# Kernel optimization log

Hardware: AMD Instinct MI355X
Metric: run time of the kernel (lower is better)

The kernel has to match this reference:

```python
import jax, jax.numpy as jnp
import numpy as np

B, D, H, K = 65536, 256, 256, 11
TEMP = 1.0
EPS = 1e-8  # torch cosine_similarity eps


def _gelu(v):
    return jax.nn.gelu(v, approximate=False)  # torch nn.GELU default is exact


def setup_inputs() -> dict:
    key = jax.random.key(0)
    ks = jax.random.split(key, 9)
    s_d = 1.0 / np.sqrt(D)
    s_h = 1.0 / np.sqrt(H)
    return {
        "x": jax.random.normal(ks[0], (B, D), jnp.float32),
        # K transform MLPs, stacked: D->H (gelu) ->D
        "Tw1": jax.random.normal(ks[1], (K, D, H), jnp.float32) * s_d,
        "Tb1": jax.random.normal(ks[2], (K, H), jnp.float32) * 0.01,
        "Tw2": jax.random.normal(ks[3], (K, H, D), jnp.float32) * s_h,
        "Tb2": jax.random.normal(ks[4], (K, D), jnp.float32) * 0.01,
        # encoder MLP: D->H (gelu) ->H
        "Ew1": jax.random.normal(ks[5], (D, H), jnp.float32) * s_d,
        "Eb1": jax.random.normal(ks[6], (H,), jnp.float32) * 0.01,
        "Ew2": jax.random.normal(ks[7], (H, H), jnp.float32) * s_h,
        "Eb2": jax.random.normal(ks[8], (H,), jnp.float32) * 0.01,
    }


def reference(x, Tw1, Tb1, Tw2, Tb2, Ew1, Eb1, Ew2, Eb2):
    def enc(h):  # [..., D] -> [..., H]; dropout is identity at inference
        return _gelu(h @ Ew1 + Eb1) @ Ew2 + Eb2

    # batched transforms: [K, B, D]
    tx = _gelu(jnp.einsum('bd,kdh->kbh', x, Tw1) + Tb1[:, None, :])
    tx = jnp.einsum('kbh,khd->kbd', tx, Tw2) + Tb2[:, None, :]

    z = enc(x)        # [B, H]
    zt = enc(tx)      # [K, B, H]

    nz = jnp.linalg.norm(z, axis=-1)    # [B]
    nzt = jnp.linalg.norm(zt, axis=-1)  # [K, B]

    # exp(cos(z, z_k) / T)  -> [K, B]
    sim_z = jnp.exp(jnp.einsum('bh,kbh->kb', z, zt)
                    / jnp.maximum(nz[None, :] * nzt, EPS) / TEMP)
    # exp(cos(z_l, z_k) / T) -> [K, K, B]
    S = jnp.exp(jnp.einsum('lbh,kbh->lkb', zt, zt)
                / jnp.maximum(nzt[:, None, :] * nzt[None, :, :], EPS) / TEMP)
    diag = jnp.diagonal(S, axis1=0, axis2=1).T  # [K, B]
    neg = S.sum(axis=0) - diag                  # sum over l != k

    scores = jnp.log(sim_z / (sim_z + neg))     # [K, B]
    return -scores.sum(axis=0)                  # [B]
```

## Files before the change

### kernel.cpp

```cpp
#include <hip/hip_runtime.h>
#include <hip/hip_bf16.h>
#include <stdint.h>

#define BTOT  65536
#define KTR   11
#define NSLOT 12

typedef __attribute__((ext_vector_type(8))) short bf16x8_t;
typedef __attribute__((ext_vector_type(4))) float f32x4_t;

__device__ __forceinline__ int act_addr(int m, int n) {
    return m * 256 + ((((n >> 3) + m) & 31) << 3) + (n & 7);
}

__device__ __forceinline__ float gelu_fast(float x) {
    float x2 = x * x;
    float t2 = 1.5957691216057308f * x * fmaf(0.044715f, x2, 1.0f);
    float e  = __expf(fminf(t2, 30.f));
    return x * e * __builtin_amdgcn_rcpf(1.0f + e);
}

__global__ void cast_x_kernel(const float* __restrict__ x, __hip_bfloat16* __restrict__ xb) {
    int i = (blockIdx.x * 256 + threadIdx.x) * 4;
    float4 v = *(const float4*)(x + i);
    union { __hip_bfloat16 h[4]; uint64_t u; } o;
    o.h[0] = __float2bfloat16(v.x);
    o.h[1] = __float2bfloat16(v.y);
    o.h[2] = __float2bfloat16(v.z);
    o.h[3] = __float2bfloat16(v.w);
    *(uint64_t*)(xb + i) = o.u;
}

__global__ void transpose_cast_kernel(const float* __restrict__ in,
                                      __hip_bfloat16* __restrict__ out,
                                      int R, int C) {
    __shared__ float tile[32][33];
    int tpc = C >> 5;
    int tr = (blockIdx.x / tpc) << 5;
    int tc = (blockIdx.x % tpc) << 5;
    const float* bi = in + (size_t)blockIdx.y * R * C;
    __hip_bfloat16* bo = out + (size_t)blockIdx.y * R * C;
    int lx = threadIdx.x & 31, ly = threadIdx.x >> 5;
    #pragma unroll
    for (int r = 0; r < 32; r += 8)
        tile[ly + r][lx] = bi[(size_t)(tr + ly + r) * C + tc + lx];
    __syncthreads();
    #pragma unroll
    for (int r = 0; r < 32; r += 8)
        bo[(size_t)(tc + ly + r) * R + tr + lx] = __float2bfloat16(tile[lx][ly + r]);
}

__global__ void fuse_w_kernel(const __hip_bfloat16* __restrict__ Ew1t,
                              const __hip_bfloat16* __restrict__ Tw2b,
                              __hip_bfloat16* __restrict__ Wft)
{
    __shared__ __align__(16) __hip_bfloat16 bt[64 * 256];
    const int tid  = threadIdx.x;
    const int wave = tid >> 6, lane = tid & 63;
    const int lr = lane & 15, q = lane >> 4;
    const int k  = blockIdx.y;
    const int h0 = blockIdx.x << 6;
    const __hip_bfloat16* src = Tw2b + (size_t)k * 65536;

    #pragma unroll
    for (int i = 0; i < 8; ++i) {
        int lin = i * 256 + tid;
        int r = lin >> 5, g = lin & 31;
        bf16x8_t v = *(const bf16x8_t*)(src + (size_t)(h0 + r) * 256 + g * 8);
        *(bf16x8_t*)(bt + act_addr(r, g * 8)) = v;
    }
    __syncthreads();

    const int wc = wave << 6;
    f32x4_t acc[4][4];
    #pragma unroll
    for (int mt = 0; mt < 4; ++mt)
        #pragma unroll
        for (int nt = 0; nt < 4; ++nt)
            acc[mt][nt] = (f32x4_t){0.f, 0.f, 0.f, 0.f};

    #pragma unroll 1
    for (int kc = 0; kc < 8; ++kc) {
        const int kof = (kc << 5) + (q << 3);
        bf16x8_t a[4], b[4];
        #pragma unroll
        for (int mt = 0; mt < 4; ++mt)
            a[mt] = *(const bf16x8_t*)(Ew1t + (size_t)(wc + (mt << 4) + lr) * 256 + kof);
        #pragma unroll
        for (int nt = 0; nt < 4; ++nt)
            b[nt] = *(const bf16x8_t*)(bt + act_addr((nt << 4) + lr, kof));
        #pragma unroll
        for (int mt = 0; mt < 4; ++mt)
            #pragma unroll
            for (int nt = 0; nt < 4; ++nt)
                acc[mt][nt] = __builtin_amdgcn_mfma_f32_16x16x32_bf16(a[mt], b[nt], acc[mt][nt], 0, 0, 0);
    }

    __hip_bfloat16* dst = Wft + (size_t)k * 65536;
    #pragma unroll
    for (int mt = 0; mt < 4; ++mt)
        #pragma unroll
        for (int nt = 0; nt < 4; ++nt) {
            const int h = h0 + (nt << 4) + lr;
            #pragma unroll
            for (int r = 0; r < 4; ++r) {
                const int j = wc + (mt << 4) + (q << 2) + r;
                dst[(size_t)j * 256 + h] = __float2bfloat16(acc[mt][nt][r]);
            }
        }
}

__global__ void fuse_b_kernel(const float* __restrict__ Tb2,
                              const float* __restrict__ Ew1,
                              const float* __restrict__ Eb1,
                              float* __restrict__ bf)
{
    const int k = blockIdx.x, j = threadIdx.x;
    float s = Eb1[j];
    #pragma unroll 4
    for (int d = 0; d < 256; ++d)
        s = fmaf(Tb2[k * 256 + d], Ew1[d * 256 + j], s);
    bf[k * 256 + j] = s;
}

__device__ void run_stage(__hip_bfloat16* act,
                          const __hip_bfloat16* __restrict__ Wt,
                          const float* __restrict__ bias,
                          bool do_gelu, int wave, int lane)
{
    const int lr = lane & 15;
    const int q  = lane >> 4;
    const int wc = wave << 6;

    f32x4_t acc[4][4];
    #pragma unroll
    for (int mt = 0; mt < 4; ++mt)
        #pragma unroll
        for (int nt = 0; nt < 4; ++nt)
            acc[mt][nt] = (f32x4_t){0.f, 0.f, 0.f, 0.f};

    bf16x8_t a[4];
    #pragma unroll
    for (int mt = 0; mt < 4; ++mt)
        a[mt] = *(const bf16x8_t*)(Wt + (size_t)(wc + (mt << 4) + lr) * 256 + (q << 3));

    #pragma unroll 1
    for (int kc = 0; kc < 8; ++kc) {
        const int kof = (kc << 5) + (q << 3);
        bf16x8_t an[4];
        if (kc < 7) {
            #pragma unroll
            for (int mt = 0; mt < 4; ++mt)
                an[mt] = *(const bf16x8_t*)(Wt + (size_t)(wc + (mt << 4) + lr) * 256 + kof + 32);
        }
        bf16x8_t b[4];
        #pragma unroll
        for (int nt = 0; nt < 4; ++nt)
            b[nt] = *(const bf16x8_t*)(act + act_addr((nt << 4) + lr, kof));
        #pragma unroll
        for (int mt = 0; mt < 4; ++mt)
            #pragma unroll
            for (int nt = 0; nt < 4; ++nt)
                acc[mt][nt] = __builtin_amdgcn_mfma_f32_16x16x32_bf16(a[mt], b[nt], acc[mt][nt], 0, 0, 0);
        if (kc < 7) {
            #pragma unroll
            for (int mt = 0; mt < 4; ++mt) a[mt] = an[mt];
        }
    }

    __syncthreads();
    #pragma unroll
    for (int mt = 0; mt < 4; ++mt) {
        const int nbase = wc + (mt << 4) + (q << 2);
        const float4 bv = *(const float4*)(bias + nbase);
        #pragma unroll
        for (int nt = 0; nt < 4; ++nt) {
            const int row = (nt << 4) + lr;
            union { __hip_bfloat16 h[4]; uint64_t u; } o;
            #pragma unroll
            for (int r = 0; r < 4; ++r) {
                float v = acc[mt][nt][r] + ((const float*)&bv)[r];
                if (do_gelu) v = gelu_fast(v);
                o.h[r] = __float2bfloat16(v);
            }
            *(uint64_t*)(act + act_addr(row, nbase)) = o.u;
        }
    }
    __syncthreads();
}

__launch_bounds__(256, 3)
__global__ void chain_kernel(const __hip_bfloat16* __restrict__ xb,
                             const __hip_bfloat16* __restrict__ Tw1t,
                             const float* __restrict__ Tb1,
                             const __hip_bfloat16* __restrict__ Wft,
                             const float* __restrict__ bfb,
                             const __hip_bfloat16* __restrict__ Ew1t,
                             const float* __restrict__ Eb1,
                             const __hip_bfloat16* __restrict__ Ew2t,
                             const float* __restrict__ Eb2,
                             __hip_bfloat16* __restrict__ zbuf,
                             int b0)
{
    __shared__ __align__(16) __hip_bfloat16 act[64 * 256];
    const int tid  = threadIdx.x;
    const int wave = tid >> 6, lane = tid & 63;
    const int slot = blockIdx.y;
    const int tile = blockIdx.x;

    #pragma unroll
    for (int i = 0; i < 8; ++i) {
        int lin = i * 256 + tid;
        int r = lin >> 5, g = lin & 31;
        bf16x8_t v = *(const bf16x8_t*)(xb + (size_t)(b0 + tile * 64 + r) * 256 + g * 8);
        *(bf16x8_t*)(act + act_addr(r, g * 8)) = v;
    }
    __syncthreads();

    if (slot < KTR) {
        run_stage(act, Tw1t + (size_t)slot * 65536, Tb1 + slot * 256, true, wave, lane);
        run_stage(act, Wft  + (size_t)slot * 65536, bfb + slot * 256, true, wave, lane);
    } else {
        run_stage(act, Ew1t, Eb1, true, wave, lane);
    }
    run_stage(act, Ew2t, Eb2, false, wave, lane);

    __hip_bfloat16* dst = zbuf + ((size_t)(tile * 64) * NSLOT + slot) * 256;
    #pragma unroll
    for (int i = 0; i < 8; ++i) {
        int lin = i * 256 + tid;
        int r = lin >> 5, g = lin & 31;
        bf16x8_t v = *(const bf16x8_t*)(act + act_addr(r, g * 8));
        *(bf16x8_t*)(dst + (size_t)r * NSLOT * 256 + g * 8) = v;
    }
}

__launch_bounds__(256, 4)
__global__ void reduce_kernel(const __hip_bfloat16* __restrict__ zbuf,
                              float* __restrict__ out, int b0, int nrows)
{
    __shared__ float Gw[4][16][17];
    const int tid  = threadIdx.x;
    const int wave = tid >> 6, lane = tid & 63;
    const int lr = lane & 15, q = lane >> 4;
    const int slot = lr < NSLOT ? lr : NSLOT - 1;
    const int nw = gridDim.x * 4;
    const size_t lanoff = (size_t)slot * 256 + (q << 3);

    #pragma unroll 1
    for (int r = blockIdx.x * 4 + wave; r < nrows; r += nw) {
        const __hip_bfloat16* zr = zbuf + (size_t)r * (NSLOT * 256) + lanoff;
        bf16x8_t v[8];
        #pragma unroll
        for (int kc = 0; kc < 8; ++kc)
            v[kc] = *(const bf16x8_t*)(zr + kc * 32);

        f32x4_t acc = (f32x4_t){0.f, 0.f, 0.f, 0.f};
        #pragma unroll
        for (int kc = 0; kc < 8; ++kc)
            acc = __builtin_amdgcn_mfma_f32_16x16x32_bf16(v[kc], v[kc], acc, 0, 0, 0);

        #pragma unroll
        for (int rr = 0; rr < 4; ++rr)
            Gw[wave][(q << 2) + rr][lr] = acc[rr];
        float term = 0.f;
        if (lane < 11) {
            const int k = lane;
            float n[NSLOT];
            #pragma unroll
            for (int l = 0; l < NSLOT; ++l) n[l] = sqrtf(Gw[wave][l][l]);
            const float nk = n[k];
            float neg = 0.f;
            #pragma unroll
            for (int l = 0; l < KTR; ++l)
                if (l != k)
                    neg += __expf(Gw[wave][l][k] / fmaxf(n[l] * nk, 1e-8f));
            float cz = Gw[wave][KTR][k] / fmaxf(n[KTR] * nk, 1e-8f);
            term = __logf(__expf(cz) + neg) - cz;
        }
        term += __shfl_xor(term, 1);
        term += __shfl_xor(term, 2);
        term += __shfl_xor(term, 4);
        term += __shfl_xor(term, 8);
        if (lane == 0) out[b0 + r] = term;
    }
}

extern "C" void kernel_launch(void* const* d_in, const int* in_sizes, int n_in,
                              void* d_out, int out_size, void* d_ws, size_t ws_size,
                              hipStream_t stream)
{
    const float* x   = (const float*)d_in[0];
    const float* Tw1 = (const float*)d_in[1];
    const float* Tb1 = (const float*)d_in[2];
    const float* Tw2 = (const float*)d_in[3];
    const float* Tb2 = (const float*)d_in[4];
    const float* Ew1 = (const float*)d_in[5];
    const float* Eb1 = (const float*)d_in[6];
    const float* Ew2 = (const float*)d_in[7];
    const float* Eb2 = (const float*)d_in[8];
    float* out = (float*)d_out;

    char* ws = (char*)d_ws;
    const size_t off_xb   = 0;
    const size_t off_tw1  = off_xb   + (size_t)BTOT * 256 * 2;
    const size_t off_wf   = off_tw1  + (size_t)KTR * 65536 * 2;
    const size_t off_ew1  = off_wf   + (size_t)KTR * 65536 * 2;
    const size_t off_ew2  = off_ew1  + (size_t)65536 * 2;
    const size_t off_tw2b = off_ew2  + (size_t)65536 * 2;
    const size_t off_bf   = off_tw2b + (size_t)KTR * 65536 * 2;
    const size_t off_z    = off_bf   + (size_t)KTR * 256 * 4;

    __hip_bfloat16* xb   = (__hip_bfloat16*)(ws + off_xb);
    __hip_bfloat16* Tw1t = (__hip_bfloat16*)(ws + off_tw1);
    __hip_bfloat16* Wft  = (__hip_bfloat16*)(ws + off_wf);
    __hip_bfloat16* Ew1t = (__hip_bfloat16*)(ws + off_ew1);
    __hip_bfloat16* Ew2t = (__hip_bfloat16*)(ws + off_ew2);
    __hip_bfloat16* Tw2b = (__hip_bfloat16*)(ws + off_tw2b);
    float*          bfb  = (float*)(ws + off_bf);
    __hip_bfloat16* zbuf = (__hip_bfloat16*)(ws + off_z);

    long long zbytes = (long long)ws_size - (long long)off_z;
    long long rows_cap = zbytes > 0 ? zbytes / ((long long)NSLOT * 256 * 2) : 0;
    int chunk = (int)((rows_cap / 128) * 128);
    if (chunk > BTOT) chunk = BTOT;
    if (chunk < 128) chunk = 128;

    cast_x_kernel<<<dim3(BTOT * 256 / 1024), 256, 0, stream>>>(x, xb);
    cast_x_kernel<<<dim3(KTR * 65536 / 1024), 256, 0, stream>>>(Tw2, Tw2b);
    transpose_cast_kernel<<<dim3(64, KTR), 256, 0, stream>>>(Tw1, Tw1t, 256, 256);
    transpose_cast_kernel<<<dim3(64, 1),   256, 0, stream>>>(Ew1, Ew1t, 256, 256);
    transpose_cast_kernel<<<dim3(64, 1),   256, 0, stream>>>(Ew2, Ew2t, 256, 256);
    fuse_b_kernel<<<dim3(KTR), 256, 0, stream>>>(Tb2, Ew1, Eb1, bfb);
    fuse_w_kernel<<<dim3(4, KTR), 256, 0, stream>>>(Ew1t, Tw2b, Wft);

    for (int b0 = 0; b0 < BTOT; b0 += chunk) {
        int rows = (BTOT - b0 < chunk) ? (BTOT - b0) : chunk;
        chain_kernel<<<dim3(rows / 64, NSLOT), 256, 0, stream>>>(
            xb, Tw1t, Tb1, Wft, bfb, Ew1t, Eb1, Ew2t, Eb2, zbuf, b0);
        reduce_kernel<<<dim3(4096), 256, 0, stream>>>(zbuf, out, b0, rows);
    }
}
```

Baseline: 893.9 us.

## Double-buffer reduce loads, fold bias into accumulator init, template gelu stage

The reduce kernel now gives each wave a fixed run of 8 rows and ping-pongs two register buffers, loading the next row while the current one is processed. The grid is sized as rows/32 instead of a grid-stride loop. In the chain kernel, bias now initialises the MFMA accumulators, the gelu flag becomes a template parameter, and gelu uses exp2 with a pre-scaled constant. The reduce kernel also multiplies by reciprocal norms instead of dividing, with a clamped epsilon, which slightly changes the epsilon semantics. Double buffering costs extra registers.

```diff
diff --git a/kernel.cpp b/kernel.cpp
--- a/kernel.cpp
+++ b/kernel.cpp
@@ -15,8 +15,8 @@
 
 __device__ __forceinline__ float gelu_fast(float x) {
     float x2 = x * x;
-    float t2 = 1.5957691216057308f * x * fmaf(0.044715f, x2, 1.0f);
-    float e  = __expf(fminf(t2, 30.f));
+    float t2 = 2.3022083f * x * fmaf(0.044715f, x2, 1.0f);
+    float e  = exp2f(fminf(t2, 44.f));
     return x * e * __builtin_amdgcn_rcpf(1.0f + e);
 }
 
@@ -123,10 +123,11 @@
     bf[k * 256 + j] = s;
 }
 
+template<bool DO_GELU>
 __device__ void run_stage(__hip_bfloat16* act,
                           const __hip_bfloat16* __restrict__ Wt,
                           const float* __restrict__ bias,
-                          bool do_gelu, int wave, int lane)
+                          int wave, int lane)
 {
     const int lr = lane & 15;
     const int q  = lane >> 4;
@@ -134,10 +135,12 @@
 
     f32x4_t acc[4][4];
     #pragma unroll
-    for (int mt = 0; mt < 4; ++mt)
+    for (int mt = 0; mt < 4; ++mt) {
+        const float4 bv = *(const float4*)(bias + wc + (mt << 4) + (q << 2));
         #pragma unroll
         for (int nt = 0; nt < 4; ++nt)
-            acc[mt][nt] = (f32x4_t){0.f, 0.f, 0.f, 0.f};
+            acc[mt][nt] = (f32x4_t){bv.x, bv.y, bv.z, bv.w};
+    }
 
     bf16x8_t a[4];
     #pragma unroll
@@ -172,15 +175,14 @@
     #pragma unroll
     for (int mt = 0; mt < 4; ++mt) {
         const int nbase = wc + (mt << 4) + (q << 2);
-        const float4 bv = *(const float4*)(bias + nbase);
         #pragma unroll
         for (int nt = 0; nt < 4; ++nt) {
             const int row = (nt << 4) + lr;
             union { __hip_bfloat16 h[4]; uint64_t u; } o;
             #pragma unroll
             for (int r = 0; r < 4; ++r) {
-                float v = acc[mt][nt][r] + ((const float*)&bv)[r];
-                if (do_gelu) v = gelu_fast(v);
+                float v = acc[mt][nt][r];
+                if (DO_GELU) v = gelu_fast(v);
                 o.h[r] = __float2bfloat16(v);
             }
             *(uint64_t*)(act + act_addr(row, nbase)) = o.u;
@@ -218,12 +220,12 @@
     __syncthreads();
 
     if (slot < KTR) {
-        run_stage(act, Tw1t + (size_t)slot * 65536, Tb1 + slot * 256, true, wave, lane);
-        run_stage(act, Wft  + (size_t)slot * 65536, bfb + slot * 256, true, wave, lane);
+        run_stage<true>(act, Tw1t + (size_t)slot * 65536, Tb1 + slot * 256, wave, lane);
+        run_stage<true>(act, Wft  + (size_t)slot * 65536, bfb + slot * 256, wave, lane);
     } else {
-        run_stage(act, Ew1t, Eb1, true, wave, lane);
-    }
-    run_stage(act, Ew2t, Eb2, false, wave, lane);
+        run_stage<true>(act, Ew1t, Eb1, wave, lane);
+    }
+    run_stage<false>(act, Ew2t, Eb2, wave, lane);
 
     __hip_bfloat16* dst = zbuf + ((size_t)(tile * 64) * NSLOT + slot) * 256;
     #pragma unroll
@@ -235,54 +237,76 @@
     }
 }
 
+#define ROW_BODY(V, I)                                                        \
+    {                                                                         \
+        f32x4_t acc = (f32x4_t){0.f, 0.f, 0.f, 0.f};                          \
+        _Pragma("unroll")                                                     \
+        for (int kc = 0; kc < 8; ++kc)                                        \
+            acc = __builtin_amdgcn_mfma_f32_16x16x32_bf16(V[kc], V[kc], acc, 0, 0, 0); \
+        _Pragma("unroll")                                                     \
+        for (int rr = 0; rr < 4; ++rr)                                        \
+            Gw[wave][(q << 2) + rr][lr] = acc[rr];                            \
+        float term = 0.f;                                                     \
+        if (lane < 11) {                                                      \
+            const int k = lane;                                               \
+            float nr[NSLOT];                                                  \
+            _Pragma("unroll")                                                 \
+            for (int l = 0; l < NSLOT; ++l)                                   \
+                nr[l] = __builtin_amdgcn_rcpf(fmaxf(sqrtf(Gw[wave][l][l]), 1e-4f)); \
+            const float nrk = nr[k];                                          \
+            float neg = 0.f;                                                  \
+            _Pragma("unroll")                                                 \
+            for (int l = 0; l < KTR; ++l)                                     \
+                if (l != k)                                                   \
+                    neg += __expf(Gw[wave][l][k] * nr[l] * nrk);              \
+            float cz = Gw[wave][KTR][k] * nr[KTR] * nrk;                      \
+            term = __logf(__expf(cz) + neg) - cz;                             \
+        }                                                                     \
+        term += __shfl_xor(term, 1);                                          \
+        term += __shfl_xor(term, 2);                                          \
+        term += __shfl_xor(term, 4);                                          \
+        term += __shfl_xor(term, 8);                                          \
+        if (lane == 0) out[b0 + r0 + (I)] = term;                             \
+    }
+
 __launch_bounds__(256, 4)
 __global__ void reduce_kernel(const __hip_bfloat16* __restrict__ zbuf,
-                              float* __restrict__ out, int b0, int nrows)
+                              float* __restrict__ out, int b0)
 {
     __shared__ float Gw[4][16][17];
     const int tid  = threadIdx.x;
     const int wave = tid >> 6, lane = tid & 63;
     const int lr = lane & 15, q = lane >> 4;
     const int slot = lr < NSLOT ? lr : NSLOT - 1;
-    const int nw = gridDim.x * 4;
     const size_t lanoff = (size_t)slot * 256 + (q << 3);
 
+    const int r0 = (blockIdx.x * 4 + wave) * 8;
+    const __hip_bfloat16* zr = zbuf + (size_t)r0 * (NSLOT * 256) + lanoff;
+
+    bf16x8_t va[8], vb[8];
+    #pragma unroll
+    for (int kc = 0; kc < 8; ++kc)
+        va[kc] = *(const bf16x8_t*)(zr + kc * 32);
+
     #pragma unroll 1
-    for (int r = blockIdx.x * 4 + wave; r < nrows; r += nw) {
-        const __hip_bfloat16* zr = zbuf + (size_t)r * (NSLOT * 256) + lanoff;
-        bf16x8_t v[8];
-        #pragma unroll
-        for (int kc = 0; kc < 8; ++kc)
-            v[kc] = *(const bf16x8_t*)(zr + kc * 32);
-
-        f32x4_t acc = (f32x4_t){0.f, 0.f, 0.f, 0.f};
-        #pragma unroll
-        for (int kc = 0; kc < 8; ++kc)
-            acc = __builtin_amdgcn_mfma_f32_16x16x32_bf16(v[kc], v[kc], acc, 0, 0, 0);
-
-        #pragma unroll
-        for (int rr = 0; rr < 4; ++rr)
-            Gw[wave][(q << 2) + rr][lr] = acc[rr];
-        float term = 0.f;
-        if (lane < 11) {
-            const int k = lane;
-            float n[NSLOT];
-            #pragma unroll
-            for (int l = 0; l < NSLOT; ++l) n[l] = sqrtf(Gw[wave][l][l]);
-            const float nk = n[k];
-            float neg = 0.f;
-            #pragma unroll
-            for (int l = 0; l < KTR; ++l)
-                if (l != k)
-                    neg += __expf(Gw[wave][l][k] / fmaxf(n[l] * nk, 1e-8f));
-            float cz = Gw[wave][KTR][k] / fmaxf(n[KTR] * nk, 1e-8f);
-            term = __logf(__expf(cz) + neg) - cz;
-        }
-        term += __shfl_xor(term, 1);
-        term += __shfl_xor(term, 2);
-        term += __shfl_xor(term, 4);
-        term += __shfl_xor(term, 8);
-        if (lane == 0) out[b0 + r] = term;
+    for (int i2 = 0; i2 < 4; ++i2) {
+        const int ie = i2 * 2;
+        {
+            const __hip_bfloat16* zn = zr + (size_t)(ie + 1) * (NSLOT * 256);
+            #pragma unroll
+            for (int kc = 0; kc < 8; ++kc)
+                vb[kc] = *(const bf16x8_t*)(zn + kc * 32);
+            ROW_BODY(va, ie)
+        }
+        {
+            if (ie + 2 < 8) {
+                const __hip_bfloat16* zn = zr + (size_t)(ie + 2) * (NSLOT * 256);
+                #pragma unroll
+                for (int kc = 0; kc < 8; ++kc)
+                    va[kc] = *(const bf16x8_t*)(zn + kc * 32);
+            }
+            ROW_BODY(vb, ie + 1)
+        }
     }
 }
 
@@ -338,6 +362,6 @@
         int rows = (BTOT - b0 < chunk) ? (BTOT - b0) : chunk;
         chain_kernel<<<dim3(rows / 64, NSLOT), 256, 0, stream>>>(
             xb, Tw1t, Tb1, Wft, bfb, Ew1t, Eb1, Ew2t, Eb2, zbuf, b0);
-        reduce_kernel<<<dim3(4096), 256, 0, stream>>>(zbuf, out, b0, rows);
-    }
-}
+        reduce_kernel<<<dim3(rows / 32), 256, 0, stream>>>(zbuf, out, b0);
+    }
+}
```

After: 871.9 us. 1.03x faster.
